# Optimization experiments

Measured on AMD Instinct MI355X. Metric: run time of the kernel, lower is better.

Reference implementation:

```python
import jax, jax.numpy as jnp
import numpy as np

B, L, F, H = 8, 1024, 1024, 16
D = F // H  # head dim = 64

def setup_inputs() -> dict:
    key = jax.random.key(0)
    k1, k2, k3, k4 = jax.random.split(key, 4)
    x = jax.random.normal(k1, (B, L, F), jnp.float32)
    # lecun_normal-style scaling for projections
    w_qkv = jax.random.normal(k2, (F, 3 * F), jnp.float32) / jnp.sqrt(F)
    # relative position bias table: (2*window-1, heads)
    rpe_table = jax.random.normal(k3, (2 * L - 1, H), jnp.float32) * 0.02
    w_out = jax.random.normal(k4, (F, F), jnp.float32) / jnp.sqrt(F)
    return {"x": x, "w_qkv": w_qkv, "rpe_table": rpe_table, "w_out": w_out}

def reference(x, w_qkv, rpe_table, w_out):
    # QKV projection (use_bias=False)
    qkv = jnp.einsum('blf,fe->ble', x, w_qkv)              # [B, L, 3F]
    qkv = qkv.reshape(B, L, H, 3 * D)
    q, k, v = jnp.split(qkv, 3, axis=-1)                   # each [B, L, H, D]
    q = q / jnp.sqrt(jnp.asarray(D, x.dtype))
    # relative positional bias: gather table at index (i - j + L - 1)
    rel_idx = jnp.arange(L)[:, None] - jnp.arange(L)[None, :] + (L - 1)  # [L, L]
    bias = jnp.transpose(rpe_table[rel_idx], (2, 0, 1))    # [H, L, L]
    scores = jnp.einsum('bqhd,bkhd->bhqk', q, k) + bias[None]  # [B, H, L, L]
    attn = jax.nn.softmax(scores, axis=-1)
    out = jnp.einsum('bhqk,bkhd->bqhd', attn, v)           # [B, L, H, D]
    out = out.reshape(B, L, F)
    return jnp.einsum('blf,fo->blo', out, w_out)
```

## Files before the change

### kernel.cpp

```cpp
#include <hip/hip_runtime.h>


typedef __attribute__((ext_vector_type(8))) short bf16x8;
typedef __attribute__((ext_vector_type(4))) float f32x4;
typedef unsigned short u16;
typedef unsigned int u32;

__device__ __forceinline__ u16 f2bf(float f) {
  u32 u = __builtin_bit_cast(u32, f);
  u = (u + 0x7fffu + ((u >> 16) & 1u)) >> 16;
  return (u16)u;
}

__device__ __forceinline__ f32x4 mfma16(bf16x8 a, bf16x8 b, f32x4 c) {
  return __builtin_amdgcn_mfma_f32_16x16x32_bf16(a, b, c, 0, 0, 0);
}

__device__ __forceinline__ void gld_lds16(const u16* g, u16* l) {
  __builtin_amdgcn_global_load_lds(
      (const __attribute__((address_space(1))) unsigned int*)g,
      (__attribute__((address_space(3))) unsigned int*)l, 16, 0, 0);
}

__global__ __launch_bounds__(256) void cast_kernel(const float* __restrict__ in,
                                                   u16* __restrict__ out, int n8) {
  int i = blockIdx.x * 256 + threadIdx.x;
  if (i >= n8) return;
  float4 a = ((const float4*)in)[2 * i];
  float4 b = ((const float4*)in)[2 * i + 1];
  uint4 o;
  o.x = (u32)f2bf(a.x) | ((u32)f2bf(a.y) << 16);
  o.y = (u32)f2bf(a.z) | ((u32)f2bf(a.w) << 16);
  o.z = (u32)f2bf(b.x) | ((u32)f2bf(b.y) << 16);
  o.w = (u32)f2bf(b.z) | ((u32)f2bf(b.w) << 16);
  ((uint4*)out)[i] = o;
}

__global__ __launch_bounds__(256) void transpose_cast_kernel(const float* __restrict__ in,
                                                             u16* __restrict__ out,
                                                             int R, int C) {
  __shared__ float tile[32][33];
  const int c0 = blockIdx.x * 32, r0 = blockIdx.y * 32;
  const int tx = threadIdx.x, ty = threadIdx.y;
#pragma unroll
  for (int i = 0; i < 32; i += 8)
    tile[ty + i][tx] = in[(size_t)(r0 + ty + i) * C + (c0 + tx)];
  __syncthreads();
#pragma unroll
  for (int i = 0; i < 32; i += 8)
    out[(size_t)(c0 + ty + i) * R + (r0 + tx)] = f2bf(tile[tx][ty + i]);
}

template <int EPI>
__global__ __launch_bounds__(256) void gemm_kernel(const u16* __restrict__ A,
                                                   const u16* __restrict__ BT,
                                                   void* __restrict__ C0,
                                                   void* __restrict__ C1,
                                                   int M, int N, int K) {
  __shared__ u16 As[128][64];
  __shared__ u16 Bs[128][64];
  const int tid = threadIdx.x;
  const int lane = tid & 63, w = tid >> 6;
  const int wrow = w >> 1, wcol = w & 1;
  const int bm0 = blockIdx.y * 128, bn0 = blockIdx.x * 128;
  const int l15 = lane & 15, l4 = lane >> 4;
  const int lr = lane >> 3, lc = (lane & 7) * 8;

  const f32x4 zero = {0.f, 0.f, 0.f, 0.f};
  f32x4 acc[4][4];
  for (int i = 0; i < 4; ++i)
    for (int j = 0; j < 4; ++j) acc[i][j] = zero;

  for (int k0 = 0; k0 < K; k0 += 64) {
    __syncthreads();
#pragma unroll
    for (int j = 0; j < 4; ++j) {
      int chunk = w * 4 + j;
      int r = chunk * 8 + lr;
      gld_lds16(A + (size_t)(bm0 + r) * K + k0 + lc, &As[0][0] + chunk * 512);
      gld_lds16(BT + (size_t)(bn0 + r) * K + k0 + lc, &Bs[0][0] + chunk * 512);
    }
    __syncthreads();
#pragma unroll
    for (int ks = 0; ks < 2; ++ks) {
      bf16x8 afr[4], bfr[4];
#pragma unroll
      for (int mi = 0; mi < 4; ++mi)
        afr[mi] = *(const bf16x8*)&As[wrow * 64 + mi * 16 + l15][ks * 32 + l4 * 8];
#pragma unroll
      for (int ni = 0; ni < 4; ++ni)
        bfr[ni] = *(const bf16x8*)&Bs[wcol * 64 + ni * 16 + l15][ks * 32 + l4 * 8];
#pragma unroll
      for (int mi = 0; mi < 4; ++mi)
#pragma unroll
        for (int ni = 0; ni < 4; ++ni)
          acc[mi][ni] = mfma16(afr[mi], bfr[ni], acc[mi][ni]);
    }
  }

  const int rbase = bm0 + wrow * 64 + l4 * 4;
  const int cbase = bn0 + wcol * 64 + l15;
  if constexpr (EPI == 1) {
    float* C = (float*)C0;
#pragma unroll
    for (int mi = 0; mi < 4; ++mi)
#pragma unroll
      for (int reg = 0; reg < 4; ++reg)
#pragma unroll
        for (int ni = 0; ni < 4; ++ni)
          C[(size_t)(rbase + mi * 16 + reg) * N + cbase + ni * 16] = acc[mi][ni][reg];
  } else {
    __syncthreads();
    u16* qkb = (u16*)C0;
    u16* vT = (u16*)C1;
    const int bq = bm0 >> 10;
    u16* buf = &As[0][0] + w * 1024;
#pragma unroll
    for (int ni = 0; ni < 4; ++ni) {
      int n16 = bn0 + wcol * 64 + ni * 16;
      int h = n16 / 192, sub = n16 - h * 192;
      if (sub < 128) {
#pragma unroll
        for (int mi = 0; mi < 4; ++mi)
#pragma unroll
          for (int reg = 0; reg < 4; ++reg) {
            int row = rbase + mi * 16 + reg;
            qkb[(size_t)row * 2048 + h * 128 + sub + l15] = f2bf(acc[mi][ni][reg]);
          }
      } else {
        asm volatile("s_waitcnt lgkmcnt(0)" ::: "memory");
#pragma unroll
        for (int mi = 0; mi < 4; ++mi)
#pragma unroll
          for (int reg = 0; reg < 4; ++reg) {
            int ml = mi * 16 + l4 * 4 + reg;
            buf[l15 * 64 + (((ml >> 3) ^ (l15 & 7)) * 8) + (ml & 7)] =
                f2bf(acc[mi][ni][reg]);
          }
        asm volatile("s_waitcnt lgkmcnt(0)" ::: "memory");
        int dbase = sub - 128;
#pragma unroll
        for (int pass = 0; pass < 2; ++pass) {
          int nl = lane >> 2, c2 = (lane & 3) + pass * 4;
          uint4 val = *(uint4*)&buf[nl * 64 + ((c2 ^ (nl & 7)) * 8)];
          int m = bm0 + wrow * 64 + c2 * 8;
          *(uint4*)&vT[(((size_t)(bq * 16 + h) * 64 + (dbase + nl)) << 10) + (m & 1023)] =
              val;
        }
      }
    }
  }
}

__global__ __launch_bounds__(256) void attn_kernel(const u16* __restrict__ qk,
                                                   const u16* __restrict__ vT,
                                                   const float* __restrict__ rpe,
                                                   u16* __restrict__ attn_out) {
  __shared__ u16 Ks[128][64];
  __shared__ u16 Vs[64][128];
  __shared__ u16 Ps[4][16][128];
  __shared__ float rpe_s[1087];

  const int tid = threadIdx.x, lane = tid & 63, w = tid >> 6;
  const int l15 = lane & 15, l4 = lane >> 4;
  const int bid = blockIdx.x;
  const int qt = bid >> 7, bh = bid & 127;
  const int h = bh & 15, b = bh >> 4;
  const int q0 = qt * 64;
  const float LOG2E = 1.44269504f;

  for (int t = tid; t < 1087; t += 256)
    rpe_s[t] = rpe[(size_t)(q0 + t) * 16 + h] * LOG2E;

  const u16* qbase = qk + ((size_t)(b * 1024 + q0 + w * 16) * 2048 + h * 128);
  bf16x8 aq[2];
#pragma unroll
  for (int ks = 0; ks < 2; ++ks)
    aq[ks] = *(const bf16x8*)(qbase + (size_t)l15 * 2048 + ks * 32 + l4 * 8);

  const f32x4 zero = {0.f, 0.f, 0.f, 0.f};
  float m_run[4], l_run[4];
  f32x4 oacc[4];
#pragma unroll
  for (int i = 0; i < 4; ++i) { m_run[i] = -1e30f; l_run[i] = 0.f; oacc[i] = zero; }

  const u16* kbase = qk + ((size_t)(b * 1024) * 2048 + h * 128 + 64);
  const u16* vbase = vT + (size_t)bh * 64 * 1024;

  for (int kt = 0; kt < 8; ++kt) {
    const int kv0 = kt * 128;
    __syncthreads();
#pragma unroll
    for (int p = 0; p < 4; ++p) {
      int r = p * 32 + (tid >> 3), c = tid & 7;
      *(uint4*)&Ks[r][(c ^ (r & 7)) * 8] =
          *(const uint4*)(kbase + (size_t)(kv0 + r) * 2048 + c * 8);
    }
#pragma unroll
    for (int p = 0; p < 4; ++p) {
      int r = p * 16 + (tid >> 4), c = tid & 15;
      *(uint4*)&Vs[r][(c ^ (r & 7)) * 8] =
          *(const uint4*)(vbase + (size_t)r * 1024 + kv0 + c * 8);
    }
    __syncthreads();

    f32x4 s[8];
    __builtin_amdgcn_s_setprio(1);
#pragma unroll
    for (int jt = 0; jt < 8; ++jt) {
      f32x4 t = zero;
#pragma unroll
      for (int ks = 0; ks < 2; ++ks) {
        bf16x8 bk = *(const bf16x8*)&Ks[jt * 16 + l15][((ks * 4 + l4) ^ (l15 & 7)) * 8];
        t = mfma16(aq[ks], bk, t);
      }
      s[jt] = t;
    }
    __builtin_amdgcn_s_setprio(0);
#pragma unroll
    for (int jt = 0; jt < 8; ++jt)
#pragma unroll
      for (int reg = 0; reg < 4; ++reg) {
        int idx = (w * 16 + l4 * 4 + reg) - (kv0 + jt * 16 + l15) + 1023;
        s[jt][reg] = s[jt][reg] * (0.125f * LOG2E) + rpe_s[idx];
      }
    float rmax[4];
    bool need = false;
#pragma unroll
    for (int reg = 0; reg < 4; ++reg) {
      float rm = fmaxf(fmaxf(s[0][reg], s[1][reg]), fmaxf(s[2][reg], s[3][reg]));
      rm = fmaxf(rm, fmaxf(fmaxf(s[4][reg], s[5][reg]), fmaxf(s[6][reg], s[7][reg])));
      rm = fmaxf(rm, __shfl_xor(rm, 1));
      rm = fmaxf(rm, __shfl_xor(rm, 2));
      rm = fmaxf(rm, __shfl_xor(rm, 4));
      rm = fmaxf(rm, __shfl_xor(rm, 8));
      rmax[reg] = rm;
      need = need || (rm > m_run[reg]);
    }
    if (__any(need)) {
#pragma unroll
      for (int reg = 0; reg < 4; ++reg) {
        float mnew = fmaxf(m_run[reg], rmax[reg]);
        float sc = __builtin_amdgcn_exp2f(m_run[reg] - mnew);
        m_run[reg] = mnew;
        l_run[reg] *= sc;
#pragma unroll
        for (int dt = 0; dt < 4; ++dt) oacc[dt][reg] *= sc;
      }
    }
#pragma unroll
    for (int reg = 0; reg < 4; ++reg) {
      float rsum = 0.f;
      int q = l4 * 4 + reg;
#pragma unroll
      for (int jt = 0; jt < 8; ++jt) {
        float pexp = __builtin_amdgcn_exp2f(s[jt][reg] - m_run[reg]);
        rsum += pexp;
        Ps[w][q][(((jt * 2 + (l15 >> 3)) ^ (q & 7)) * 8) + (l15 & 7)] = f2bf(pexp);
      }
      rsum += __shfl_xor(rsum, 1);
      rsum += __shfl_xor(rsum, 2);
      rsum += __shfl_xor(rsum, 4);
      rsum += __shfl_xor(rsum, 8);
      l_run[reg] += rsum;
    }
    __builtin_amdgcn_s_setprio(1);
#pragma unroll
    for (int ksv = 0; ksv < 4; ++ksv) {
      bf16x8 pa = *(const bf16x8*)&Ps[w][l15][((ksv * 4 + l4) ^ (l15 & 7)) * 8];
#pragma unroll
      for (int dt = 0; dt < 4; ++dt) {
        bf16x8 vb = *(const bf16x8*)&Vs[dt * 16 + l15][((ksv * 4 + l4) ^ (l15 & 7)) * 8];
        oacc[dt] = mfma16(pa, vb, oacc[dt]);
      }
    }
    __builtin_amdgcn_s_setprio(0);
  }

#pragma unroll
  for (int reg = 0; reg < 4; ++reg) {
    float inv = 1.f / l_run[reg];
    int row = b * 1024 + q0 + w * 16 + l4 * 4 + reg;
#pragma unroll
    for (int dt = 0; dt < 4; ++dt)
      attn_out[(size_t)row * 1024 + h * 64 + dt * 16 + l15] = f2bf(oacc[dt][reg] * inv);
  }
}

extern "C" void kernel_launch(void* const* d_in, const int* in_sizes, int n_in,
                              void* d_out, int out_size, void* d_ws, size_t ws_size,
                              hipStream_t stream) {
  const float* x     = (const float*)d_in[0];
  const float* w_qkv = (const float*)d_in[1];
  const float* rpe   = (const float*)d_in[2];
  const float* w_out = (const float*)d_in[3];

  char* ws = (char*)d_ws;
  u16* xb    = (u16*)(ws);
  u16* attnb = (u16*)(ws);
  u16* wqkvT = (u16*)(ws + 16777216);
  u16* woutT = (u16*)(ws + 23068672);
  u16* qkbuf = (u16*)(ws + 25165824);
  u16* vTbuf = (u16*)(ws + 58720256);

  cast_kernel<<<4096, 256, 0, stream>>>(x, xb, 8192 * 1024 / 8);
  dim3 tb(32, 8);
  transpose_cast_kernel<<<dim3(3072 / 32, 1024 / 32), tb, 0, stream>>>(w_qkv, wqkvT, 1024, 3072);
  transpose_cast_kernel<<<dim3(1024 / 32, 1024 / 32), tb, 0, stream>>>(w_out, woutT, 1024, 1024);

  gemm_kernel<0><<<dim3(3072 / 128, 8192 / 128), 256, 0, stream>>>(
      xb, wqkvT, (void*)qkbuf, (void*)vTbuf, 8192, 3072, 1024);

  attn_kernel<<<2048, 256, 0, stream>>>(qkbuf, vTbuf, rpe, attnb);

  gemm_kernel<1><<<dim3(1024 / 128, 8192 / 128), 256, 0, stream>>>(
      attnb, woutT, d_out, nullptr, 8192, 1024, 1024);
}
```

Measured before the change: 298.9 us.

## Restructure attention: 128-query blocks, transposed S layout, async K/V LDS loads

The attention kernel now runs 512 threads per block over 128 queries, so each K/V tile loaded into LDS serves twice as many queries. The score MFMA operands are swapped so each lane holds one query column, which replaces the per-row shuffle reductions with two cross-group shuffles and keeps a single running max and sum per lane. K/V tiles are copied with direct global-to-LDS loads, and probabilities are packed with v_cvt_pk_bf16_f32. The RPE table is pre-transposed and pre-scaled by a small new kernel, whose output reuses the w_out-transpose workspace region, so that transpose is moved after attention; this adds a dependency on launch order.

```diff
diff --git a/kernel.cpp b/kernel.cpp
--- a/kernel.cpp
+++ b/kernel.cpp
@@ -49,6 +49,13 @@
 #pragma unroll
   for (int i = 0; i < 32; i += 8)
     out[(size_t)(c0 + ty + i) * R + (r0 + tx)] = f2bf(tile[tx][ty + i]);
+}
+
+__global__ __launch_bounds__(256) void rpe_prep_kernel(const float* __restrict__ rpe,
+                                                       float* __restrict__ rpeT) {
+  int o = blockIdx.x * 256 + threadIdx.x;
+  int h = o >> 11, i = o & 2047;
+  if (i < 2047) rpeT[h * 2048 + i] = rpe[(size_t)i * 16 + h] * 1.44269504f;
 }
 
 template <int EPI>
@@ -152,55 +159,50 @@
   }
 }
 
-__global__ __launch_bounds__(256) void attn_kernel(const u16* __restrict__ qk,
-                                                   const u16* __restrict__ vT,
-                                                   const float* __restrict__ rpe,
-                                                   u16* __restrict__ attn_out) {
+__global__ __launch_bounds__(512, 4) void attn_kernel(const u16* __restrict__ qk,
+                                                      const u16* __restrict__ vT,
+                                                      const float* __restrict__ rpeT,
+                                                      u16* __restrict__ attn_out) {
   __shared__ u16 Ks[128][64];
   __shared__ u16 Vs[64][128];
-  __shared__ u16 Ps[4][16][128];
-  __shared__ float rpe_s[1087];
+  __shared__ u16 Ps[8][16][128];
+  __shared__ float rpe_s[1152];
 
   const int tid = threadIdx.x, lane = tid & 63, w = tid >> 6;
   const int l15 = lane & 15, l4 = lane >> 4;
   const int bid = blockIdx.x;
   const int qt = bid >> 7, bh = bid & 127;
   const int h = bh & 15, b = bh >> 4;
-  const int q0 = qt * 64;
-  const float LOG2E = 1.44269504f;
-
-  for (int t = tid; t < 1087; t += 256)
-    rpe_s[t] = rpe[(size_t)(q0 + t) * 16 + h] * LOG2E;
-
-  const u16* qbase = qk + ((size_t)(b * 1024 + q0 + w * 16) * 2048 + h * 128);
-  bf16x8 aq[2];
-#pragma unroll
-  for (int ks = 0; ks < 2; ++ks)
-    aq[ks] = *(const bf16x8*)(qbase + (size_t)l15 * 2048 + ks * 32 + l4 * 8);
+  const int q0 = qt * 128;
+
+  for (int t = tid; t < 1151; t += 512)
+    rpe_s[t] = rpeT[h * 2048 + q0 + t];
+
+  const u16* qbase = qk + ((size_t)(b * 1024 + q0 + w * 16 + l15) * 2048 + h * 128);
+  bf16x8 bq0 = *(const bf16x8*)(qbase + l4 * 8);
+  bf16x8 bq1 = *(const bf16x8*)(qbase + 32 + l4 * 8);
 
   const f32x4 zero = {0.f, 0.f, 0.f, 0.f};
-  float m_run[4], l_run[4];
+  float m_run = -1e30f, l_run = 0.f;
   f32x4 oacc[4];
 #pragma unroll
-  for (int i = 0; i < 4; ++i) { m_run[i] = -1e30f; l_run[i] = 0.f; oacc[i] = zero; }
-
-  const u16* kbase = qk + ((size_t)(b * 1024) * 2048 + h * 128 + 64);
-  const u16* vbase = vT + (size_t)bh * 64 * 1024;
+  for (int i = 0; i < 4; ++i) oacc[i] = zero;
+
+  const u16* kgbase = qk + ((size_t)(b * 1024) * 2048 + h * 128 + 64);
+  const u16* vgbase = vT + (size_t)bh * 65536;
 
   for (int kt = 0; kt < 8; ++kt) {
     const int kv0 = kt * 128;
     __syncthreads();
 #pragma unroll
-    for (int p = 0; p < 4; ++p) {
-      int r = p * 32 + (tid >> 3), c = tid & 7;
-      *(uint4*)&Ks[r][(c ^ (r & 7)) * 8] =
-          *(const uint4*)(kbase + (size_t)(kv0 + r) * 2048 + c * 8);
-    }
-#pragma unroll
-    for (int p = 0; p < 4; ++p) {
-      int r = p * 16 + (tid >> 4), c = tid & 15;
-      *(uint4*)&Vs[r][(c ^ (r & 7)) * 8] =
-          *(const uint4*)(vbase + (size_t)r * 1024 + kv0 + c * 8);
+    for (int p = 0; p < 2; ++p) {
+      int e = p * 512 + tid;
+      int kr = e >> 3, kc = e & 7;
+      gld_lds16(kgbase + (size_t)(kv0 + kr) * 2048 + ((kc ^ (kr & 7)) * 8),
+                &Ks[0][0] + (size_t)(p * 512 + w * 64) * 8);
+      int vr = e >> 4, vc = e & 15;
+      gld_lds16(vgbase + (size_t)vr * 1024 + kv0 + ((vc ^ (vr & 7)) * 8),
+                &Vs[0][0] + (size_t)(p * 512 + w * 64) * 8);
     }
     __syncthreads();
 
@@ -209,61 +211,61 @@
 #pragma unroll
     for (int jt = 0; jt < 8; ++jt) {
       f32x4 t = zero;
-#pragma unroll
-      for (int ks = 0; ks < 2; ++ks) {
-        bf16x8 bk = *(const bf16x8*)&Ks[jt * 16 + l15][((ks * 4 + l4) ^ (l15 & 7)) * 8];
-        t = mfma16(aq[ks], bk, t);
+      bf16x8 ak0 = *(const bf16x8*)&Ks[jt * 16 + l15][((l4) ^ (l15 & 7)) * 8];
+      bf16x8 ak1 = *(const bf16x8*)&Ks[jt * 16 + l15][((4 + l4) ^ (l15 & 7)) * 8];
+      t = mfma16(ak0, bq0, t);
+      t = mfma16(ak1, bq1, t);
+      s[jt] = t;
+    }
+    __builtin_amdgcn_s_setprio(0);
+
+    const int ibase = w * 16 + l15 + 1023 - kv0 - l4 * 4;
+#pragma unroll
+    for (int jt = 0; jt < 8; ++jt)
+#pragma unroll
+      for (int reg = 0; reg < 4; ++reg)
+        s[jt][reg] = s[jt][reg] * (0.125f * 1.44269504f) + rpe_s[ibase - jt * 16 - reg];
+
+    float rm = fmaxf(fmaxf(s[0][0], s[0][1]), fmaxf(s[0][2], s[0][3]));
+#pragma unroll
+    for (int jt = 1; jt < 8; ++jt)
+      rm = fmaxf(rm, fmaxf(fmaxf(s[jt][0], s[jt][1]), fmaxf(s[jt][2], s[jt][3])));
+    rm = fmaxf(rm, __shfl_xor(rm, 16));
+    rm = fmaxf(rm, __shfl_xor(rm, 32));
+
+    if (__any(rm > m_run)) {
+      float mnew = fmaxf(m_run, rm);
+      float sc = __builtin_amdgcn_exp2f(m_run - mnew);
+      m_run = mnew;
+      l_run *= sc;
+#pragma unroll
+      for (int reg = 0; reg < 4; ++reg) {
+        float scr = __shfl(sc, l4 * 4 + reg);
+#pragma unroll
+        for (int dt = 0; dt < 4; ++dt) oacc[dt][reg] *= scr;
       }
-      s[jt] = t;
-    }
-    __builtin_amdgcn_s_setprio(0);
-#pragma unroll
-    for (int jt = 0; jt < 8; ++jt)
-#pragma unroll
-      for (int reg = 0; reg < 4; ++reg) {
-        int idx = (w * 16 + l4 * 4 + reg) - (kv0 + jt * 16 + l15) + 1023;
-        s[jt][reg] = s[jt][reg] * (0.125f * LOG2E) + rpe_s[idx];
-      }
-    float rmax[4];
-    bool need = false;
-#pragma unroll
-    for (int reg = 0; reg < 4; ++reg) {
-      float rm = fmaxf(fmaxf(s[0][reg], s[1][reg]), fmaxf(s[2][reg], s[3][reg]));
-      rm = fmaxf(rm, fmaxf(fmaxf(s[4][reg], s[5][reg]), fmaxf(s[6][reg], s[7][reg])));
-      rm = fmaxf(rm, __shfl_xor(rm, 1));
-      rm = fmaxf(rm, __shfl_xor(rm, 2));
-      rm = fmaxf(rm, __shfl_xor(rm, 4));
-      rm = fmaxf(rm, __shfl_xor(rm, 8));
-      rmax[reg] = rm;
-      need = need || (rm > m_run[reg]);
-    }
-    if (__any(need)) {
-#pragma unroll
-      for (int reg = 0; reg < 4; ++reg) {
-        float mnew = fmaxf(m_run[reg], rmax[reg]);
-        float sc = __builtin_amdgcn_exp2f(m_run[reg] - mnew);
-        m_run[reg] = mnew;
-        l_run[reg] *= sc;
-#pragma unroll
-        for (int dt = 0; dt < 4; ++dt) oacc[dt][reg] *= sc;
-      }
-    }
-#pragma unroll
-    for (int reg = 0; reg < 4; ++reg) {
-      float rsum = 0.f;
-      int q = l4 * 4 + reg;
-#pragma unroll
-      for (int jt = 0; jt < 8; ++jt) {
-        float pexp = __builtin_amdgcn_exp2f(s[jt][reg] - m_run[reg]);
-        rsum += pexp;
-        Ps[w][q][(((jt * 2 + (l15 >> 3)) ^ (q & 7)) * 8) + (l15 & 7)] = f2bf(pexp);
-      }
-      rsum += __shfl_xor(rsum, 1);
-      rsum += __shfl_xor(rsum, 2);
-      rsum += __shfl_xor(rsum, 4);
-      rsum += __shfl_xor(rsum, 8);
-      l_run[reg] += rsum;
-    }
+    }
+
+    float rsum = 0.f;
+#pragma unroll
+    for (int jt = 0; jt < 8; ++jt) {
+      float p0 = __builtin_amdgcn_exp2f(s[jt][0] - m_run);
+      float p1 = __builtin_amdgcn_exp2f(s[jt][1] - m_run);
+      float p2 = __builtin_amdgcn_exp2f(s[jt][2] - m_run);
+      float p3 = __builtin_amdgcn_exp2f(s[jt][3] - m_run);
+      rsum += (p0 + p1) + (p2 + p3);
+      u32 pk01, pk23;
+      asm("v_cvt_pk_bf16_f32 %0, %1, %2" : "=v"(pk01) : "v"(p0), "v"(p1));
+      asm("v_cvt_pk_bf16_f32 %0, %1, %2" : "=v"(pk23) : "v"(p2), "v"(p3));
+      int chunk = (jt * 2 + (l4 >> 1)) ^ (l15 & 7);
+      u32* dst = (u32*)&Ps[w][l15][chunk * 8 + (l4 & 1) * 4];
+      dst[0] = pk01;
+      dst[1] = pk23;
+    }
+    rsum += __shfl_xor(rsum, 16);
+    rsum += __shfl_xor(rsum, 32);
+    l_run += rsum;
+
     __builtin_amdgcn_s_setprio(1);
 #pragma unroll
     for (int ksv = 0; ksv < 4; ++ksv) {
@@ -277,13 +279,14 @@
     __builtin_amdgcn_s_setprio(0);
   }
 
+  float inv = 1.f / l_run;
 #pragma unroll
   for (int reg = 0; reg < 4; ++reg) {
-    float inv = 1.f / l_run[reg];
+    float invr = __shfl(inv, l4 * 4 + reg);
     int row = b * 1024 + q0 + w * 16 + l4 * 4 + reg;
 #pragma unroll
     for (int dt = 0; dt < 4; ++dt)
-      attn_out[(size_t)row * 1024 + h * 64 + dt * 16 + l15] = f2bf(oacc[dt][reg] * inv);
+      attn_out[(size_t)row * 1024 + h * 64 + dt * 16 + l15] = f2bf(oacc[dt][reg] * invr);
   }
 }
 
@@ -300,18 +303,21 @@
   u16* attnb = (u16*)(ws);
   u16* wqkvT = (u16*)(ws + 16777216);
   u16* woutT = (u16*)(ws + 23068672);
+  float* rpeT = (float*)(ws + 23068672);
   u16* qkbuf = (u16*)(ws + 25165824);
   u16* vTbuf = (u16*)(ws + 58720256);
 
   cast_kernel<<<4096, 256, 0, stream>>>(x, xb, 8192 * 1024 / 8);
   dim3 tb(32, 8);
   transpose_cast_kernel<<<dim3(3072 / 32, 1024 / 32), tb, 0, stream>>>(w_qkv, wqkvT, 1024, 3072);
-  transpose_cast_kernel<<<dim3(1024 / 32, 1024 / 32), tb, 0, stream>>>(w_out, woutT, 1024, 1024);
+  rpe_prep_kernel<<<128, 256, 0, stream>>>(rpe, rpeT);
 
   gemm_kernel<0><<<dim3(3072 / 128, 8192 / 128), 256, 0, stream>>>(
       xb, wqkvT, (void*)qkbuf, (void*)vTbuf, 8192, 3072, 1024);
 
-  attn_kernel<<<2048, 256, 0, stream>>>(qkbuf, vTbuf, rpe, attnb);
+  attn_kernel<<<1024, 512, 0, stream>>>(qkbuf, vTbuf, rpeT, attnb);
+
+  transpose_cast_kernel<<<dim3(1024 / 32, 1024 / 32), tb, 0, stream>>>(w_out, woutT, 1024, 1024);
 
   gemm_kernel<1><<<dim3(1024 / 128, 8192 / 128), 256, 0, stream>>>(
       attnb, woutT, d_out, nullptr, 8192, 1024, 1024);
```

Measured after the change: 267.8 us. 1.12x faster.
